# Kernel optimization log

Hardware: AMD Instinct MI355X
Metric: run time of the kernel (lower is better)

## Reference

```python
import jax, jax.numpy as jnp
import numpy as np

SIGMA = 45.0
N, M, D = 4096, 4096, 1024


def setup_inputs() -> dict:
    key = jax.random.key(0)
    k1, k2 = jax.random.split(key)
    inputs = jax.random.normal(k1, (N, D), dtype=jnp.float32)
    samples = jax.random.normal(k2, (M, D), dtype=jnp.float32)
    return {"inputs": inputs, "samples": samples}


def _sq_dists(x, y):
    # ||x_i||^2 + ||y_j||^2 - 2 x_i.y_j  -> [N, M]
    prod = x @ y.T
    xs = jnp.sum(x * x, axis=1)[:, None]
    ys = jnp.sum(y * y, axis=1)[None, :]
    return xs + ys - 2.0 * prod


def reference(inputs, samples):
    n = inputs.shape[0]
    m = samples.shape[0]
    x = inputs.reshape(n, -1)
    y = samples.reshape(m, -1)
    inv_s2 = 1.0 / (SIGMA ** 2)

    k_xx = _sq_dists(x, x)
    k_yy = _sq_dists(y, y)
    k_xy = _sq_dists(x, y)

    # unbiased MMD: exclude diagonal terms of k_xx, k_yy
    exx = jnp.exp(-k_xx * inv_s2)
    eyy = jnp.exp(-k_yy * inv_s2)
    exy = jnp.exp(-k_xy * inv_s2)

    mmd = (jnp.sum(exx) - jnp.sum(jnp.exp(-jnp.diag(k_xx) * inv_s2))) / (n * (n - 1))
    mmd = mmd + (jnp.sum(eyy) - jnp.sum(jnp.exp(-jnp.diag(k_yy) * inv_s2))) / (m * (m - 1))
    mmd = mmd - 2.0 / (n * m) * jnp.sum(exy)
    return mmd
```

## Files before the change

kernel.cpp:

```cpp
#include <hip/hip_runtime.h>
#include <math.h>


typedef _Float16 f16_t;
typedef _Float16 f16x4 __attribute__((ext_vector_type(4)));
typedef _Float16 f16x8 __attribute__((ext_vector_type(8)));
typedef float floatx4 __attribute__((ext_vector_type(4)));

#define NROWS 4096
#define MROWS 4096
#define DDIM  1024
#define BM    128
#define BK    32
#define TILE  (BM * BK)
#define NT    (NROWS / BM)
#define TRI   (NT * (NT + 1) / 2)
#define NBLK  (2 * TRI + NT * NT)

__global__ __launch_bounds__(256) void convert_kernel(
    const float* __restrict__ X, const float* __restrict__ Y,
    f16_t* __restrict__ Xh, f16_t* __restrict__ Yh,
    float* __restrict__ nx, float* __restrict__ ny) {
    const int wid  = threadIdx.x >> 6;
    const int lane = threadIdx.x & 63;
    const int row  = blockIdx.x * 4 + wid;
    const float* src;
    f16_t* dst;
    float* nrm;
    int r;
    if (row < NROWS) {
        r = row;         src = X + (size_t)r * DDIM;
        dst = Xh + (size_t)r * DDIM;  nrm = nx;
    } else {
        r = row - NROWS; src = Y + (size_t)r * DDIM;
        dst = Yh + (size_t)r * DDIM;  nrm = ny;
    }
    const float4* s4 = (const float4*)src;
    f16x4* d4 = (f16x4*)dst;
    float s = 0.f;
    #pragma unroll
    for (int c = 0; c < 4; c++) {
        float4 v = s4[c * 64 + lane];
        f16x4 h;
        h[0] = (f16_t)v.x; h[1] = (f16_t)v.y;
        h[2] = (f16_t)v.z; h[3] = (f16_t)v.w;
        d4[c * 64 + lane] = h;
        float h0 = (float)h[0], h1 = (float)h[1];
        float h2 = (float)h[2], h3 = (float)h[3];
        s += h0 * h0 + h1 * h1 + h2 * h2 + h3 * h3;
    }
    #pragma unroll
    for (int off = 32; off > 0; off >>= 1) s += __shfl_down(s, off);
    if (lane == 0) nrm[r] = s;
}

__global__ __launch_bounds__(256) void mmd_mfma(
    const f16_t* __restrict__ Xh, const f16_t* __restrict__ Yh,
    const float* __restrict__ nx, const float* __restrict__ ny,
    double* __restrict__ partials) {
    __shared__ __align__(16) f16_t lds[2 * TILE];
    __shared__ double wred[4];

    const int b = blockIdx.x;
    const f16_t *A, *B;
    const float *nA, *nB;
    int tr, tc;
    double coef;
    if (b < 2 * TRI) {
        int u = (b < TRI) ? b : b - TRI;
        int r = 0;
        while (u >= NT - r) { u -= NT - r; r++; }
        tr = r; tc = r + u;
        double w = (tr == tc) ? 1.0 : 2.0;
        if (b < TRI) { A = Xh; B = Xh; nA = nx; nB = nx;
                       coef = w / ((double)NROWS * (double)(NROWS - 1)); }
        else         { A = Yh; B = Yh; nA = ny; nB = ny;
                       coef = w / ((double)MROWS * (double)(MROWS - 1)); }
    } else {
        int u = b - 2 * TRI;
        tr = u / NT; tc = u % NT;
        A = Xh; B = Yh; nA = nx; nB = ny;
        coef = -2.0 / ((double)NROWS * (double)MROWS);
    }

    const int t    = threadIdx.x;
    const int wave = t >> 6;
    const int lane = t & 63;
    const int wm   = wave >> 1;
    const int wn   = wave & 1;

    const f16_t* Abase = A + (size_t)tr * BM * DDIM;
    const f16_t* Bbase = B + (size_t)tc * BM * DDIM;
    const int lrow = lane >> 2;
    const int schunk = (lane & 3) ^ ((lrow ^ (lrow >> 2)) & 3);
    const f16_t* gsrc[4];
    int ldsoff[4];
    #pragma unroll
    for (int i = 0; i < 4; i++) {
        int idx = wave * 4 + i;
        int tile = idx >> 3;
        int rg   = idx & 7;
        const f16_t* base = tile ? Bbase : Abase;
        gsrc[i] = base + (size_t)(rg * 16 + lrow) * DDIM + schunk * 8;
        ldsoff[i] = tile * TILE + rg * 16 * BK;
    }

    const int m    = lane & 15;
    const int quad = lane >> 4;
    const int ac   = quad ^ ((m ^ (m >> 2)) & 3);

    float na[16], nb[4];
    #pragma unroll
    for (int i = 0; i < 4; i++) {
        #pragma unroll
        for (int r = 0; r < 4; r++)
            na[i * 4 + r] = nA[tr * BM + wm * 64 + i * 16 + quad * 4 + r];
        nb[i] = nB[tc * BM + wn * 64 + i * 16 + m];
    }

    floatx4 acc_r[4][4];
    #pragma unroll
    for (int i = 0; i < 4; i++)
        #pragma unroll
        for (int j = 0; j < 4; j++) acc_r[i][j] = (floatx4){0.f, 0.f, 0.f, 0.f};

    for (int k0 = 0; k0 < DDIM; k0 += BK) {
        __syncthreads();
        #pragma unroll
        for (int i = 0; i < 4; i++) {
            __builtin_amdgcn_global_load_lds(
                (const __attribute__((address_space(1))) void*)(gsrc[i] + k0),
                (__attribute__((address_space(3))) void*)(lds + ldsoff[i]),
                16, 0, 0);
        }
        __syncthreads();

        f16x8 ah[4], bh[4];
        #pragma unroll
        for (int s = 0; s < 4; s++) {
            int arow = wm * 64 + s * 16 + m;
            int brow = wn * 64 + s * 16 + m;
            ah[s] = *(const f16x8*)&lds[arow * BK + ac * 8];
            bh[s] = *(const f16x8*)&lds[TILE + brow * BK + ac * 8];
        }
        #pragma unroll
        for (int i = 0; i < 4; i++)
            #pragma unroll
            for (int j = 0; j < 4; j++)
                acc_r[i][j] = __builtin_amdgcn_mfma_f32_16x16x32_f16(ah[i], bh[j], acc_r[i][j], 0, 0, 0);
    }

    const float inv_s2 = 1.0f / 2025.0f;
    float lsum = 0.f;
    #pragma unroll
    for (int i = 0; i < 4; i++)
        #pragma unroll
        for (int j = 0; j < 4; j++)
            #pragma unroll
            for (int r = 0; r < 4; r++) {
                float arg = (2.f * acc_r[i][j][r] - na[i * 4 + r] - nb[j]) * inv_s2;
                lsum += __expf(arg);
            }

    double d = (double)lsum;
    #pragma unroll
    for (int off = 32; off > 0; off >>= 1) d += __shfl_down(d, off);
    if (lane == 0) wred[wave] = d;
    __syncthreads();
    if (t == 0)
        partials[b] = (wred[0] + wred[1] + wred[2] + wred[3]) * coef;
}

__global__ __launch_bounds__(256) void final_reduce(const double* __restrict__ partials,
                                                    float* __restrict__ out) {
    __shared__ double red[256];
    int t = threadIdx.x;
    double s = 0.0;
    for (int i = t; i < NBLK; i += 256) s += partials[i];
    red[t] = s;
    __syncthreads();
    for (int off = 128; off > 0; off >>= 1) {
        if (t < off) red[t] += red[t + off];
        __syncthreads();
    }
    if (t == 0) {
        double mmd = red[0] - 1.0 / (double)(NROWS - 1) - 1.0 / (double)(MROWS - 1);
        out[0] = (float)mmd;
    }
}

extern "C" void kernel_launch(void* const* d_in, const int* in_sizes, int n_in,
                              void* d_out, int out_size, void* d_ws, size_t ws_size,
                              hipStream_t stream) {
    const float* X = (const float*)d_in[0];
    const float* Y = (const float*)d_in[1];
    float* out = (float*)d_out;

    char* p = (char*)d_ws;
    double* partials = (double*)p;            p += ((size_t)NBLK * sizeof(double) + 255) & ~255ULL;
    float* nx = (float*)p;                    p += (size_t)NROWS * sizeof(float);
    float* ny = (float*)p;                    p += (size_t)MROWS * sizeof(float);
    f16_t* Xh = (f16_t*)p;                    p += (size_t)NROWS * DDIM * sizeof(f16_t);
    f16_t* Yh = (f16_t*)p;

    convert_kernel<<<(NROWS + MROWS) / 4, 256, 0, stream>>>(X, Y, Xh, Yh, nx, ny);
    mmd_mfma<<<NBLK, 256, 0, stream>>>(Xh, Yh, nx, ny, partials);
    final_reduce<<<1, 256, 0, stream>>>(partials, out);
}
```

Before: 166.7 us.

## Use 256x128 tiles, 8 waves and 4-slot async LDS prefetch pipeline

Changes the MFMA tile to 256x128 with 512 threads (8 waves), and replaces the per-step load-then-sync loop with a 4-slot ring of LDS buffers filled three steps ahead by async global_load_lds, gated by vmcnt waits and barriers. It also remaps the symmetric XX/YY triangular blocks onto the rectangular tile grid, with weights for off-diagonal tiles, and uses setprio around the MFMA block. The aim is to hide global-load latency behind compute and raise the compute-to-load ratio. The cost is 96KB of LDS per block, which limits occupancy, and more redundant work on the diagonal tiles.

```diff
diff --git a/kernel.cpp b/kernel.cpp
--- a/kernel.cpp
+++ b/kernel.cpp
@@ -10,12 +10,14 @@
 #define NROWS 4096
 #define MROWS 4096
 #define DDIM  1024
-#define BM    128
+#define BM    256
+#define BN    128
 #define BK    32
-#define TILE  (BM * BK)
-#define NT    (NROWS / BM)
-#define TRI   (NT * (NT + 1) / 2)
-#define NBLK  (2 * TRI + NT * NT)
+#define NKT   (DDIM / BK)
+#define NTR   (NROWS / BM)
+#define NTC   (NROWS / BN)
+#define XXB   272
+#define NBLK  (2 * XXB + NTR * NTC)
 
 __global__ __launch_bounds__(256) void convert_kernel(
     const float* __restrict__ X, const float* __restrict__ Y,
@@ -54,121 +56,134 @@
     if (lane == 0) nrm[r] = s;
 }
 
-__global__ __launch_bounds__(256) void mmd_mfma(
+#define STAGE(tt_) do {                                                        \
+    const int slot_ = (tt_) & 3;                                               \
+    const int kk_ = (((tt_) < NKT) ? (tt_) : (NKT - 1)) * BK;                  \
+    __builtin_amdgcn_global_load_lds(                                          \
+        (const __attribute__((address_space(1))) void*)(gA + kk_),             \
+        (__attribute__((address_space(3))) void*)(&ldsA[slot_][wave * 1024]),  \
+        16, 0, 0);                                                             \
+    __builtin_amdgcn_global_load_lds(                                          \
+        (const __attribute__((address_space(1))) void*)(gA + kk_ + 16 * DDIM), \
+        (__attribute__((address_space(3))) void*)(&ldsA[slot_][wave * 1024 + 512]), \
+        16, 0, 0);                                                             \
+    __builtin_amdgcn_global_load_lds(                                          \
+        (const __attribute__((address_space(1))) void*)(gB + kk_),             \
+        (__attribute__((address_space(3))) void*)(&ldsB[slot_][wave * 512]),   \
+        16, 0, 0);                                                             \
+  } while (0)
+
+__global__ __launch_bounds__(512, 2) void mmd_mfma(
     const f16_t* __restrict__ Xh, const f16_t* __restrict__ Yh,
     const float* __restrict__ nx, const float* __restrict__ ny,
     double* __restrict__ partials) {
-    __shared__ __align__(16) f16_t lds[2 * TILE];
-    __shared__ double wred[4];
+    __shared__ __align__(16) f16_t ldsA[4][BM * BK];
+    __shared__ __align__(16) f16_t ldsB[4][BN * BK];
+    __shared__ double wred[8];
 
     const int b = blockIdx.x;
-    const f16_t *A, *B;
-    const float *nA, *nB;
-    int tr, tc;
+    const f16_t *Aptr, *Bptr;
+    const float *nAp, *nBp;
     double coef;
-    if (b < 2 * TRI) {
-        int u = (b < TRI) ? b : b - TRI;
-        int r = 0;
-        while (u >= NT - r) { u -= NT - r; r++; }
-        tr = r; tc = r + u;
-        double w = (tr == tc) ? 1.0 : 2.0;
-        if (b < TRI) { A = Xh; B = Xh; nA = nx; nB = nx;
-                       coef = w / ((double)NROWS * (double)(NROWS - 1)); }
-        else         { A = Yh; B = Yh; nA = ny; nB = ny;
-                       coef = w / ((double)MROWS * (double)(MROWS - 1)); }
+    if (b < 2 * XXB) {
+        int u = (b < XXB) ? b : b - XXB;
+        int i = 0;
+        while (u >= NTC - 2 * i) { u -= NTC - 2 * i; i++; }
+        const int ti = i, tj = 2 * i + u;
+        const double w = (tj >= 2 * i + 2) ? 2.0 : 1.0;
+        const f16_t* base;
+        const float* nb_;
+        double denom;
+        if (b < XXB) { base = Xh; nb_ = nx; denom = (double)NROWS * (double)(NROWS - 1); }
+        else         { base = Yh; nb_ = ny; denom = (double)MROWS * (double)(MROWS - 1); }
+        Aptr = base + (size_t)ti * BM * DDIM;
+        Bptr = base + (size_t)tj * BN * DDIM;
+        nAp = nb_ + ti * BM;  nBp = nb_ + tj * BN;
+        coef = w / denom;
     } else {
-        int u = b - 2 * TRI;
-        tr = u / NT; tc = u % NT;
-        A = Xh; B = Yh; nA = nx; nB = ny;
+        const int u = b - 2 * XXB;
+        const int ti = u >> 5, tj = u & 31;
+        Aptr = Xh + (size_t)ti * BM * DDIM;
+        Bptr = Yh + (size_t)tj * BN * DDIM;
+        nAp = nx + ti * BM;  nBp = ny + tj * BN;
         coef = -2.0 / ((double)NROWS * (double)MROWS);
     }
 
-    const int t    = threadIdx.x;
-    const int wave = t >> 6;
-    const int lane = t & 63;
+    const int tid  = threadIdx.x;
+    const int wave = tid >> 6;
+    const int lane = tid & 63;
     const int wm   = wave >> 1;
     const int wn   = wave & 1;
-
-    const f16_t* Abase = A + (size_t)tr * BM * DDIM;
-    const f16_t* Bbase = B + (size_t)tc * BM * DDIM;
-    const int lrow = lane >> 2;
-    const int schunk = (lane & 3) ^ ((lrow ^ (lrow >> 2)) & 3);
-    const f16_t* gsrc[4];
-    int ldsoff[4];
-    #pragma unroll
-    for (int i = 0; i < 4; i++) {
-        int idx = wave * 4 + i;
-        int tile = idx >> 3;
-        int rg   = idx & 7;
-        const f16_t* base = tile ? Bbase : Abase;
-        gsrc[i] = base + (size_t)(rg * 16 + lrow) * DDIM + schunk * 8;
-        ldsoff[i] = tile * TILE + rg * 16 * BK;
-    }
-
     const int m    = lane & 15;
     const int quad = lane >> 4;
-    const int ac   = quad ^ ((m ^ (m >> 2)) & 3);
-
-    float na[16], nb[4];
-    #pragma unroll
-    for (int i = 0; i < 4; i++) {
-        #pragma unroll
-        for (int r = 0; r < 4; r++)
-            na[i * 4 + r] = nA[tr * BM + wm * 64 + i * 16 + quad * 4 + r];
-        nb[i] = nB[tc * BM + wn * 64 + i * 16 + m];
-    }
-
-    floatx4 acc_r[4][4];
+    const int sw8  = (quad ^ ((m >> 1) & 3)) * 8;
+    const int aoff = (wm * 64 + m) * BK + sw8;
+    const int boff = (wn * 64 + m) * BK + sw8;
+
+    const int lr = lane >> 2;
+    const int lc = (lane & 3) ^ ((lane >> 3) & 3);
+    const f16_t* gA = Aptr + (size_t)(wave * 32 + lr) * DDIM + lc * 8;
+    const f16_t* gB = Bptr + (size_t)(wave * 16 + lr) * DDIM + lc * 8;
+
+    floatx4 acc[4][4];
     #pragma unroll
     for (int i = 0; i < 4; i++)
         #pragma unroll
-        for (int j = 0; j < 4; j++) acc_r[i][j] = (floatx4){0.f, 0.f, 0.f, 0.f};
-
-    for (int k0 = 0; k0 < DDIM; k0 += BK) {
-        __syncthreads();
-        #pragma unroll
-        for (int i = 0; i < 4; i++) {
-            __builtin_amdgcn_global_load_lds(
-                (const __attribute__((address_space(1))) void*)(gsrc[i] + k0),
-                (__attribute__((address_space(3))) void*)(lds + ldsoff[i]),
-                16, 0, 0);
+        for (int j = 0; j < 4; j++) acc[i][j] = (floatx4){0.f, 0.f, 0.f, 0.f};
+
+    STAGE(0); STAGE(1); STAGE(2);
+    asm volatile("s_waitcnt vmcnt(6)" ::: "memory");
+    __builtin_amdgcn_s_barrier();
+
+    for (int t = 0; t < NKT; ++t) {
+        const int slot = t & 3;
+        f16x8 ah[4], bh[4];
+        #pragma unroll
+        for (int s = 0; s < 4; s++) {
+            ah[s] = *(const f16x8*)&ldsA[slot][aoff + s * 16 * BK];
+            bh[s] = *(const f16x8*)&ldsB[slot][boff + s * 16 * BK];
         }
-        __syncthreads();
-
-        f16x8 ah[4], bh[4];
-        #pragma unroll
-        for (int s = 0; s < 4; s++) {
-            int arow = wm * 64 + s * 16 + m;
-            int brow = wn * 64 + s * 16 + m;
-            ah[s] = *(const f16x8*)&lds[arow * BK + ac * 8];
-            bh[s] = *(const f16x8*)&lds[TILE + brow * BK + ac * 8];
-        }
+        STAGE(t + 3);
+        asm volatile("s_waitcnt vmcnt(6)" ::: "memory");
+        __builtin_amdgcn_s_barrier();
+        __builtin_amdgcn_s_setprio(1);
         #pragma unroll
         for (int i = 0; i < 4; i++)
             #pragma unroll
             for (int j = 0; j < 4; j++)
-                acc_r[i][j] = __builtin_amdgcn_mfma_f32_16x16x32_f16(ah[i], bh[j], acc_r[i][j], 0, 0, 0);
+                acc[i][j] = __builtin_amdgcn_mfma_f32_16x16x32_f16(ah[i], bh[j], acc[i][j], 0, 0, 0);
+        __builtin_amdgcn_s_setprio(0);
+        __builtin_amdgcn_s_barrier();
     }
 
     const float inv_s2 = 1.0f / 2025.0f;
+    float nbv[4];
+    #pragma unroll
+    for (int j = 0; j < 4; j++) nbv[j] = nBp[wn * 64 + j * 16 + m];
     float lsum = 0.f;
     #pragma unroll
-    for (int i = 0; i < 4; i++)
+    for (int i = 0; i < 4; i++) {
+        floatx4 na4 = *(const floatx4*)&nAp[wm * 64 + i * 16 + quad * 4];
         #pragma unroll
         for (int j = 0; j < 4; j++)
             #pragma unroll
             for (int r = 0; r < 4; r++) {
-                float arg = (2.f * acc_r[i][j][r] - na[i * 4 + r] - nb[j]) * inv_s2;
+                float arg = (2.f * acc[i][j][r] - na4[r] - nbv[j]) * inv_s2;
                 lsum += __expf(arg);
             }
+    }
 
     double d = (double)lsum;
     #pragma unroll
     for (int off = 32; off > 0; off >>= 1) d += __shfl_down(d, off);
     if (lane == 0) wred[wave] = d;
     __syncthreads();
-    if (t == 0)
-        partials[b] = (wred[0] + wred[1] + wred[2] + wred[3]) * coef;
+    if (tid == 0) {
+        double s = 0.0;
+        #pragma unroll
+        for (int w = 0; w < 8; w++) s += wred[w];
+        partials[b] = s * coef;
+    }
 }
 
 __global__ __launch_bounds__(256) void final_reduce(const double* __restrict__ partials,
@@ -204,6 +219,6 @@
     f16_t* Yh = (f16_t*)p;
 
     convert_kernel<<<(NROWS + MROWS) / 4, 256, 0, stream>>>(X, Y, Xh, Yh, nx, ny);
-    mmd_mfma<<<NBLK, 256, 0, stream>>>(Xh, Yh, nx, ny, partials);
+    mmd_mfma<<<NBLK, 512, 0, stream>>>(Xh, Yh, nx, ny, partials);
     final_reduce<<<1, 256, 0, stream>>>(partials, out);
 }
```

New measurement: 181.2 us. 1.09x slower.

## Pack f16 operands in K-panel layout, remap blocks, fuse final reduction via atomics

Applied to the files above, without the earlier changes.

The convert kernel now writes the f16 copies as K-panels of 4096 rows by 32 columns, so each per-k-step tile load reads one contiguous chunk instead of rows strided by D. Block IDs are permuted with an (id&7)*(NBLK/8) + (id>>3) mapping, which interleaves workloads across XCDs and changes cache locality. The separate final-reduce launch is removed in favour of a double atomicAdd plus a completion counter, and the last block writes the output. This saves one launch and improves load coalescing, at the cost of atomic contention and a floating-point summation order that varies from run to run.

```diff
diff --git a/kernel.cpp b/kernel.cpp
--- a/kernel.cpp
+++ b/kernel.cpp
@@ -13,30 +13,33 @@
 #define BM    128
 #define BK    32
 #define TILE  (BM * BK)
+#define NKT   (DDIM / BK)
+#define PSTRIDE (4096 * BK)
 #define NT    (NROWS / BM)
 #define TRI   (NT * (NT + 1) / 2)
 #define NBLK  (2 * TRI + NT * NT)
 
 __global__ __launch_bounds__(256) void convert_kernel(
     const float* __restrict__ X, const float* __restrict__ Y,
-    f16_t* __restrict__ Xh, f16_t* __restrict__ Yh,
-    float* __restrict__ nx, float* __restrict__ ny) {
+    f16_t* __restrict__ Xp, f16_t* __restrict__ Yp,
+    float* __restrict__ nx, float* __restrict__ ny,
+    double* __restrict__ gsum, int* __restrict__ gcnt) {
+    if (blockIdx.x == 0 && threadIdx.x == 0) { *gsum = 0.0; *gcnt = 0; }
     const int wid  = threadIdx.x >> 6;
     const int lane = threadIdx.x & 63;
     const int row  = blockIdx.x * 4 + wid;
     const float* src;
-    f16_t* dst;
+    f16_t* dstp;
     float* nrm;
     int r;
     if (row < NROWS) {
         r = row;         src = X + (size_t)r * DDIM;
-        dst = Xh + (size_t)r * DDIM;  nrm = nx;
+        dstp = Xp;  nrm = nx;
     } else {
         r = row - NROWS; src = Y + (size_t)r * DDIM;
-        dst = Yh + (size_t)r * DDIM;  nrm = ny;
+        dstp = Yp;  nrm = ny;
     }
     const float4* s4 = (const float4*)src;
-    f16x4* d4 = (f16x4*)dst;
     float s = 0.f;
     #pragma unroll
     for (int c = 0; c < 4; c++) {
@@ -44,7 +47,8 @@
         f16x4 h;
         h[0] = (f16_t)v.x; h[1] = (f16_t)v.y;
         h[2] = (f16_t)v.z; h[3] = (f16_t)v.w;
-        d4[c * 64 + lane] = h;
+        *(f16x4*)(dstp + (size_t)(c * 8 + (lane >> 3)) * PSTRIDE
+                       + (size_t)r * BK + (lane & 7) * 4) = h;
         float h0 = (float)h[0], h1 = (float)h[1];
         float h2 = (float)h[2], h3 = (float)h[3];
         s += h0 * h0 + h1 * h1 + h2 * h2 + h3 * h3;
@@ -55,14 +59,16 @@
 }
 
 __global__ __launch_bounds__(256) void mmd_mfma(
-    const f16_t* __restrict__ Xh, const f16_t* __restrict__ Yh,
+    const f16_t* __restrict__ Xp, const f16_t* __restrict__ Yp,
     const float* __restrict__ nx, const float* __restrict__ ny,
-    double* __restrict__ partials) {
+    double* __restrict__ gsum, int* __restrict__ gcnt,
+    float* __restrict__ out) {
     __shared__ __align__(16) f16_t lds[2 * TILE];
     __shared__ double wred[4];
 
-    const int b = blockIdx.x;
-    const f16_t *A, *B;
+    const int b = ((blockIdx.x & 7) * (NBLK / 8)) + (blockIdx.x >> 3);
+
+    const f16_t *Ap, *Bp;
     const float *nA, *nB;
     int tr, tc;
     double coef;
@@ -72,14 +78,14 @@
         while (u >= NT - r) { u -= NT - r; r++; }
         tr = r; tc = r + u;
         double w = (tr == tc) ? 1.0 : 2.0;
-        if (b < TRI) { A = Xh; B = Xh; nA = nx; nB = nx;
+        if (b < TRI) { Ap = Xp; Bp = Xp; nA = nx; nB = nx;
                        coef = w / ((double)NROWS * (double)(NROWS - 1)); }
-        else         { A = Yh; B = Yh; nA = ny; nB = ny;
+        else         { Ap = Yp; Bp = Yp; nA = ny; nB = ny;
                        coef = w / ((double)MROWS * (double)(MROWS - 1)); }
     } else {
         int u = b - 2 * TRI;
-        tr = u / NT; tc = u % NT;
-        A = Xh; B = Yh; nA = nx; nB = ny;
+        tr = u >> 5; tc = u & 31;
+        Ap = Xp; Bp = Yp; nA = nx; nB = ny;
         coef = -2.0 / ((double)NROWS * (double)MROWS);
     }
 
@@ -89,8 +95,6 @@
     const int wm   = wave >> 1;
     const int wn   = wave & 1;
 
-    const f16_t* Abase = A + (size_t)tr * BM * DDIM;
-    const f16_t* Bbase = B + (size_t)tc * BM * DDIM;
     const int lrow = lane >> 2;
     const int schunk = (lane & 3) ^ ((lrow ^ (lrow >> 2)) & 3);
     const f16_t* gsrc[4];
@@ -100,8 +104,9 @@
         int idx = wave * 4 + i;
         int tile = idx >> 3;
         int rg   = idx & 7;
-        const f16_t* base = tile ? Bbase : Abase;
-        gsrc[i] = base + (size_t)(rg * 16 + lrow) * DDIM + schunk * 8;
+        const f16_t* base = tile ? (Bp + (size_t)tc * BM * BK)
+                                 : (Ap + (size_t)tr * BM * BK);
+        gsrc[i] = base + (size_t)(rg * 16 + lrow) * BK + schunk * 8;
         ldsoff[i] = tile * TILE + rg * 16 * BK;
     }
 
@@ -124,12 +129,13 @@
         #pragma unroll
         for (int j = 0; j < 4; j++) acc_r[i][j] = (floatx4){0.f, 0.f, 0.f, 0.f};
 
-    for (int k0 = 0; k0 < DDIM; k0 += BK) {
+    for (int kt = 0; kt < NKT; kt++) {
+        const size_t ko = (size_t)kt * PSTRIDE;
         __syncthreads();
         #pragma unroll
         for (int i = 0; i < 4; i++) {
             __builtin_amdgcn_global_load_lds(
-                (const __attribute__((address_space(1))) void*)(gsrc[i] + k0),
+                (const __attribute__((address_space(1))) void*)(gsrc[i] + ko),
                 (__attribute__((address_space(3))) void*)(lds + ldsoff[i]),
                 16, 0, 0);
         }
@@ -167,25 +173,16 @@
     for (int off = 32; off > 0; off >>= 1) d += __shfl_down(d, off);
     if (lane == 0) wred[wave] = d;
     __syncthreads();
-    if (t == 0)
-        partials[b] = (wred[0] + wred[1] + wred[2] + wred[3]) * coef;
-}
-
-__global__ __launch_bounds__(256) void final_reduce(const double* __restrict__ partials,
-                                                    float* __restrict__ out) {
-    __shared__ double red[256];
-    int t = threadIdx.x;
-    double s = 0.0;
-    for (int i = t; i < NBLK; i += 256) s += partials[i];
-    red[t] = s;
-    __syncthreads();
-    for (int off = 128; off > 0; off >>= 1) {
-        if (t < off) red[t] += red[t + off];
-        __syncthreads();
-    }
     if (t == 0) {
-        double mmd = red[0] - 1.0 / (double)(NROWS - 1) - 1.0 / (double)(MROWS - 1);
-        out[0] = (float)mmd;
+        double part = (wred[0] + wred[1] + wred[2] + wred[3]) * coef;
+        atomicAdd(gsum, part);
+        asm volatile("s_waitcnt vmcnt(0)" ::: "memory");
+        int old = atomicAdd(gcnt, 1);
+        if (old == NBLK - 1) {
+            double s = atomicAdd(gsum, 0.0);
+            out[0] = (float)(s - 1.0 / (double)(NROWS - 1)
+                               - 1.0 / (double)(MROWS - 1));
+        }
     }
 }
 
@@ -197,13 +194,13 @@
     float* out = (float*)d_out;
 
     char* p = (char*)d_ws;
-    double* partials = (double*)p;            p += ((size_t)NBLK * sizeof(double) + 255) & ~255ULL;
+    double* gsum = (double*)p;
+    int* gcnt = (int*)(p + sizeof(double));   p += 256;
     float* nx = (float*)p;                    p += (size_t)NROWS * sizeof(float);
     float* ny = (float*)p;                    p += (size_t)MROWS * sizeof(float);
-    f16_t* Xh = (f16_t*)p;                    p += (size_t)NROWS * DDIM * sizeof(f16_t);
-    f16_t* Yh = (f16_t*)p;
-
-    convert_kernel<<<(NROWS + MROWS) / 4, 256, 0, stream>>>(X, Y, Xh, Yh, nx, ny);
-    mmd_mfma<<<NBLK, 256, 0, stream>>>(Xh, Yh, nx, ny, partials);
-    final_reduce<<<1, 256, 0, stream>>>(partials, out);
+    f16_t* Xp = (f16_t*)p;                    p += (size_t)NROWS * DDIM * sizeof(f16_t);
+    f16_t* Yp = (f16_t*)p;
+
+    convert_kernel<<<(NROWS + MROWS) / 4, 256, 0, stream>>>(X, Y, Xp, Yp, nx, ny, gsum, gcnt);
+    mmd_mfma<<<NBLK, 256, 0, stream>>>(Xp, Yp, nx, ny, gsum, gcnt, out);
 }
```

Measured after the change: 180.1 us. 8.1% more time.
